# Kernel optimization log

Measured on AMD Instinct MI355X. Metric: run time of the kernel, lower is better.

The kernel has to match this reference:

```python
import jax, jax.numpy as jnp
import numpy as np

N_SRNA, N_MRNA, F, H, E, Q = 20000, 100000, 128, 128, 1000000, 500000


def _sage(x_src, x_dst, src_idx, dst_idx, n_dst, Wl, bl, Wr):
    # PyG SAGEConv: out = lin_l(mean_{j in N(i)} x_j) + lin_r(x_i)
    msg = x_src[src_idx]                                   # [E, F] gather
    agg = jax.ops.segment_sum(msg, dst_idx, num_segments=n_dst)
    cnt = jax.ops.segment_sum(jnp.ones((msg.shape[0],), msg.dtype), dst_idx,
                              num_segments=n_dst)
    mean = agg / jnp.maximum(cnt, 1.0)[:, None]            # [n_dst, F]
    return mean @ Wl + bl + x_dst @ Wr


def setup_inputs() -> dict:
    key = jax.random.key(0)
    ks = jax.random.split(key, 24)
    s = 1.0 / np.sqrt(F)
    inp = {
        'x_srna': jax.random.normal(ks[0], (N_SRNA, F), jnp.float32),
        'x_mrna': jax.random.normal(ks[1], (N_MRNA, F), jnp.float32),
        'src_sm': jax.random.randint(ks[2], (E,), 0, N_SRNA, jnp.int32),
        'dst_sm': jax.random.randint(ks[3], (E,), 0, N_MRNA, jnp.int32),
        'src_ms': jax.random.randint(ks[4], (E,), 0, N_MRNA, jnp.int32),
        'dst_ms': jax.random.randint(ks[5], (E,), 0, N_SRNA, jnp.int32),
        'lbl_row': jax.random.randint(ks[6], (Q,), 0, N_SRNA, jnp.int32),
        'lbl_col': jax.random.randint(ks[7], (Q,), 0, N_MRNA, jnp.int32),
    }
    wnames = ['W1l_sm', 'W1r_sm', 'W1l_ms', 'W1r_ms',
              'W2l_sm', 'W2r_sm', 'W2l_ms', 'W2r_ms']
    for i, n in enumerate(wnames):
        inp[n] = jax.random.normal(ks[8 + i], (F, H), jnp.float32) * s
    for n in ['b1_sm', 'b1_ms', 'b2_sm', 'b2_ms']:
        inp[n] = jnp.zeros((H,), jnp.float32)
    return inp


def reference(x_srna, x_mrna, src_sm, dst_sm, src_ms, dst_ms, lbl_row, lbl_col,
              W1l_sm, b1_sm, W1r_sm, W1l_ms, b1_ms, W1r_ms,
              W2l_sm, b2_sm, W2r_sm, W2l_ms, b2_ms, W2r_ms):
    # Layer 1 (hetero: each dst type receives from exactly one edge type) + ReLU
    h_mrna = jax.nn.relu(_sage(x_srna, x_mrna, src_sm, dst_sm, N_MRNA,
                               W1l_sm, b1_sm, W1r_sm))
    h_srna = jax.nn.relu(_sage(x_mrna, x_srna, src_ms, dst_ms, N_SRNA,
                               W1l_ms, b1_ms, W1r_ms))
    # Layer 2 (no activation)
    z_mrna = _sage(h_srna, h_mrna, src_sm, dst_sm, N_MRNA, W2l_sm, b2_sm, W2r_sm)
    z_srna = _sage(h_mrna, h_srna, src_ms, dst_ms, N_SRNA, W2l_ms, b2_ms, W2r_ms)
    # Edge decoder: dot product over gathered embeddings
    return jnp.sum(z_srna[lbl_row] * z_mrna[lbl_col], axis=-1)
```

## Files before the change

### kernel.cpp

```cpp
#include <hip/hip_runtime.h>

#define N_SRNA  20000
#define N_MRNA  100000
#define FDIM    128
#define NE      1000000
#define NQ      500000
#define NDST_ALL (N_MRNA + N_SRNA)

#define NB_M 196
#define NB_S 157
#define NB   (NB_M + NB_S)
#define NB_Q 196
#define ECAP 8192
#define QCAP 4096

typedef __attribute__((ext_vector_type(8))) short bf16x8;
typedef __attribute__((ext_vector_type(4))) float f32x4;

__device__ __forceinline__ unsigned short f2bf(float f) {
    unsigned int u = __float_as_uint(f);
    unsigned int r = (u + 0x7fffu + ((u >> 16) & 1u)) >> 16;
    return (unsigned short)r;
}
__device__ __forceinline__ float bf2f(unsigned short h) {
    return __uint_as_float((unsigned int)h << 16);
}

__global__ __launch_bounds__(256) void k_bscatter(const int* __restrict__ src_sm,
                                                  const int* __restrict__ dst_sm,
                                                  const int* __restrict__ src_ms,
                                                  const int* __restrict__ dst_ms,
                                                  int* __restrict__ bcur,
                                                  unsigned int* __restrict__ recs) {
    __shared__ int lh[NB], gb[NB], lc[NB];
    int t = threadIdx.x;
    for (int i = t; i < NB; i += 256) { lh[i] = 0; lc[i] = 0; }
    __syncthreads();
    unsigned int rec[16];
    int bk[16];
    int i0 = blockIdx.x * 4096;
#pragma unroll
    for (int j = 0; j < 16; ++j) {
        int i = i0 + j * 256 + t;
        int b = -1; unsigned int r = 0;
        if (i < NE) {
            int d = dst_sm[i];
            b = d >> 9;
            r = ((unsigned int)(d - (b << 9)) << 17) | (unsigned int)src_sm[i];
        } else if (i < 2 * NE) {
            int jj = i - NE;
            int d = dst_ms[jj];
            int bs = d >> 7;
            b = NB_M + bs;
            r = ((unsigned int)(d - (bs << 7)) << 17) | (unsigned int)src_ms[jj];
        }
        bk[j] = b; rec[j] = r;
        if (b >= 0) atomicAdd(&lh[b], 1);
    }
    __syncthreads();
    for (int i = t; i < NB; i += 256)
        gb[i] = lh[i] ? atomicAdd(&bcur[i], lh[i]) : 0;
    __syncthreads();
#pragma unroll
    for (int j = 0; j < 16; ++j) {
        int b = bk[j];
        if (b >= 0) {
            int slot = atomicAdd(&lc[b], 1);
            recs[(size_t)b * ECAP + gb[b] + slot] = rec[j];
        }
    }
}

__global__ __launch_bounds__(256) void k_bbuild(const unsigned int* __restrict__ recs,
                                                const int* __restrict__ bcur,
                                                int* __restrict__ begd,
                                                int* __restrict__ degd,
                                                int* __restrict__ col) {
    __shared__ int lh[512], lptr[512], lps[256];
    const int b = blockIdx.x, t = threadIdx.x;
    const int nd = (b < NB_M) ? min(512, N_MRNA - (b << 9))
                              : min(128, N_SRNA - ((b - NB_M) << 7));
    const int dst0 = (b < NB_M) ? (b << 9) : N_MRNA + ((b - NB_M) << 7);
    const int base = b * ECAP;
    const int nbe = bcur[b];

    lh[t] = 0; lh[t + 256] = 0;
    __syncthreads();
    for (int e = t; e < nbe; e += 256)
        atomicAdd(&lh[recs[(size_t)base + e] >> 17], 1);
    __syncthreads();

    int a0 = lh[2 * t], a1 = lh[2 * t + 1];
    int ps = a0 + a1;
    lps[t] = ps;
    __syncthreads();
    for (int off = 1; off < 256; off <<= 1) {
        int x = (t >= off) ? lps[t - off] : 0;
        __syncthreads();
        lps[t] += x;
        __syncthreads();
    }
    int ex = lps[t] - ps;
    lptr[2 * t] = ex;
    lptr[2 * t + 1] = ex + a0;
    __syncthreads();

    for (int d = t; d < nd; d += 256) {
        begd[dst0 + d] = base + lptr[d];
        degd[dst0 + d] = lh[d];
    }
    __syncthreads();
    lh[t] = lptr[t]; lh[t + 256] = lptr[t + 256];
    __syncthreads();
    for (int e = t; e < nbe; e += 256) {
        unsigned int r = recs[(size_t)base + e];
        int slot = atomicAdd(&lh[r >> 17], 1);
        col[base + slot] = (int)(r & 0x1FFFFu);
    }
}

__global__ __launch_bounds__(256) void k_qscatter(const int* __restrict__ lbl_row,
                                                  const int* __restrict__ lbl_col,
                                                  int* __restrict__ qbcur,
                                                  uint2* __restrict__ qrecs) {
    __shared__ int lh[NB_Q], gb[NB_Q], lc[NB_Q];
    int t = threadIdx.x;
    for (int i = t; i < NB_Q; i += 256) { lh[i] = 0; lc[i] = 0; }
    __syncthreads();
    uint2 rec[16];
    int bk[16];
    int i0 = blockIdx.x * 4096;
#pragma unroll
    for (int j = 0; j < 16; ++j) {
        int i = i0 + j * 256 + t;
        int b = -1; uint2 r = make_uint2(0, 0);
        if (i < NQ) {
            int c = lbl_col[i];
            b = c >> 9;
            r.x = (unsigned int)i;
            r.y = ((unsigned int)(c - (b << 9)) << 15) | (unsigned int)lbl_row[i];
        }
        bk[j] = b; rec[j] = r;
        if (b >= 0) atomicAdd(&lh[b], 1);
    }
    __syncthreads();
    for (int i = t; i < NB_Q; i += 256)
        gb[i] = lh[i] ? atomicAdd(&qbcur[i], lh[i]) : 0;
    __syncthreads();
#pragma unroll
    for (int j = 0; j < 16; ++j) {
        int b = bk[j];
        if (b >= 0) {
            int slot = atomicAdd(&lc[b], 1);
            qrecs[(size_t)b * QCAP + gb[b] + slot] = rec[j];
        }
    }
}

__global__ __launch_bounds__(256) void k_qbbuild(const uint2* __restrict__ qrecs,
                                                 const int* __restrict__ qbcur,
                                                 int* __restrict__ qbeg,
                                                 int* __restrict__ qdeg,
                                                 uint2* __restrict__ qdat) {
    __shared__ int lh[512], lptr[512], lps[256];
    const int b = blockIdx.x, t = threadIdx.x;
    const int nd = min(512, N_MRNA - (b << 9));
    const int col0 = b << 9;
    const int base = b * QCAP;
    const int nbe = qbcur[b];

    lh[t] = 0; lh[t + 256] = 0;
    __syncthreads();
    for (int e = t; e < nbe; e += 256)
        atomicAdd(&lh[qrecs[(size_t)base + e].y >> 15], 1);
    __syncthreads();

    int a0 = lh[2 * t], a1 = lh[2 * t + 1];
    int ps = a0 + a1;
    lps[t] = ps;
    __syncthreads();
    for (int off = 1; off < 256; off <<= 1) {
        int x = (t >= off) ? lps[t - off] : 0;
        __syncthreads();
        lps[t] += x;
        __syncthreads();
    }
    int ex = lps[t] - ps;
    lptr[2 * t] = ex;
    lptr[2 * t + 1] = ex + a0;
    __syncthreads();

    for (int d = t; d < nd; d += 256) {
        qbeg[col0 + d] = base + lptr[d];
        qdeg[col0 + d] = lh[d];
    }
    __syncthreads();
    lh[t] = lptr[t]; lh[t + 256] = lptr[t + 256];
    __syncthreads();
    for (int e = t; e < nbe; e += 256) {
        uint2 r = qrecs[(size_t)base + e];
        int slot = atomicAdd(&lh[r.y >> 15], 1);
        qdat[base + slot] = make_uint2(r.y & 0x7FFFu, r.x);
    }
}

__global__ __launch_bounds__(256) void k_cvt_bf(const float* __restrict__ src,
                                                unsigned short* __restrict__ dst, int n4) {
    int i = blockIdx.x * 256 + threadIdx.x;
    int stride = gridDim.x * 256;
    for (; i < n4; i += stride) {
        float4 v = ((const float4*)src)[i];
        unsigned int p0 = (unsigned int)f2bf(v.x) | ((unsigned int)f2bf(v.y) << 16);
        unsigned int p1 = (unsigned int)f2bf(v.z) | ((unsigned int)f2bf(v.w) << 16);
        ((uint2*)dst)[i] = make_uint2(p0, p1);
    }
}

__global__ __launch_bounds__(256) void k_build_wt4(
        const float* __restrict__ Wl0, const float* __restrict__ Wr0, unsigned short* __restrict__ Wt0,
        const float* __restrict__ Wl1, const float* __restrict__ Wr1, unsigned short* __restrict__ Wt1,
        const float* __restrict__ Wl2, const float* __restrict__ Wr2, unsigned short* __restrict__ Wt2,
        const float* __restrict__ Wl3, const float* __restrict__ Wr3, unsigned short* __restrict__ Wt3) {
    int g = blockIdx.x >> 7;
    const float* Wl; const float* Wr; unsigned short* Wt;
    if (g == 0)      { Wl = Wl0; Wr = Wr0; Wt = Wt0; }
    else if (g == 1) { Wl = Wl1; Wr = Wr1; Wt = Wt1; }
    else if (g == 2) { Wl = Wl2; Wr = Wr2; Wt = Wt2; }
    else             { Wl = Wl3; Wr = Wr3; Wt = Wt3; }
    int tid = (blockIdx.x & 127) * 256 + threadIdx.x;
    int c = tid & 127, k = tid >> 7;
    float v = (k < 128) ? Wl[k * 128 + c] : Wr[(k - 128) * 128 + c];
    Wt[c * 256 + k] = f2bf(v);
}

__global__ __launch_bounds__(256) void k_seg_mean2(const unsigned short* __restrict__ srcA,
                                                   const unsigned short* __restrict__ srcB,
                                                   const int* __restrict__ begd,
                                                   const int* __restrict__ degd,
                                                   const int* __restrict__ cols,
                                                   unsigned short* __restrict__ outA,
                                                   unsigned short* __restrict__ outB,
                                                   int nA, int nTot) {
    int wave = (blockIdx.x * 256 + threadIdx.x) >> 6;
    int l = threadIdx.x & 63;
    if (wave >= nTot) return;
    const int q = l >> 4, lq = l & 15;
    const unsigned short* xs;
    unsigned short* o;
    if (wave < nA) { xs = srcA; o = outA + (size_t)wave * FDIM; }
    else           { xs = srcB; o = outB + (size_t)(wave - nA) * FDIM; }

    int beg = begd[wave], deg = degd[wave];
    float acc[8];
#pragma unroll
    for (int k = 0; k < 8; ++k) acc[k] = 0.f;

    int e = 0;
    for (; e + 8 <= deg; e += 8) {
        int s0 = cols[beg + e + q];
        int s1 = cols[beg + e + 4 + q];
        bf16x8 v0 = *(const bf16x8*)(xs + (size_t)s0 * FDIM + lq * 8);
        bf16x8 v1 = *(const bf16x8*)(xs + (size_t)s1 * FDIM + lq * 8);
#pragma unroll
        for (int k = 0; k < 8; ++k) acc[k] += bf2f((unsigned short)v0[k]);
#pragma unroll
        for (int k = 0; k < 8; ++k) acc[k] += bf2f((unsigned short)v1[k]);
    }
    for (; e < deg; e += 4) {
        bool valid = (e + q) < deg;
        int idx = beg + min(e + q, max(deg - 1, 0));
        int s = cols[idx];
        bf16x8 v = *(const bf16x8*)(xs + (size_t)s * FDIM + lq * 8);
        if (valid) {
#pragma unroll
            for (int k = 0; k < 8; ++k) acc[k] += bf2f((unsigned short)v[k]);
        }
    }
#pragma unroll
    for (int k = 0; k < 8; ++k) {
        acc[k] += __shfl_xor(acc[k], 16);
        acc[k] += __shfl_xor(acc[k], 32);
    }
    if (q == 0) {
        float inv = 1.0f / fmaxf((float)deg, 1.0f);
        uint4 pv;
        pv.x = (unsigned int)f2bf(acc[0] * inv) | ((unsigned int)f2bf(acc[1] * inv) << 16);
        pv.y = (unsigned int)f2bf(acc[2] * inv) | ((unsigned int)f2bf(acc[3] * inv) << 16);
        pv.z = (unsigned int)f2bf(acc[4] * inv) | ((unsigned int)f2bf(acc[5] * inv) << 16);
        pv.w = (unsigned int)f2bf(acc[6] * inv) | ((unsigned int)f2bf(acc[7] * inv) << 16);
        ((uint4*)o)[lq] = pv;
    }
}

template <bool RELU>
__global__ __launch_bounds__(256, 2) void k_gemm_mfma2(
        const unsigned short* __restrict__ A0a, const unsigned short* __restrict__ A1a,
        const unsigned short* __restrict__ Wta, const float* __restrict__ biasa,
        unsigned short* __restrict__ outa, int na, int nblka,
        const unsigned short* __restrict__ A0b, const unsigned short* __restrict__ A1b,
        const unsigned short* __restrict__ Wtb, const float* __restrict__ biasb,
        unsigned short* __restrict__ outb, int nb) {
    __shared__ uint4 smem4[4352];
    char* smem = (char*)smem4;

    const unsigned short *A0, *A1, *Wt;
    const float* bias;
    unsigned short* out;
    int n, bid;
    if ((int)blockIdx.x < nblka) {
        A0 = A0a; A1 = A1a; Wt = Wta; bias = biasa; out = outa; n = na; bid = blockIdx.x;
    } else {
        A0 = A0b; A1 = A1b; Wt = Wtb; bias = biasb; out = outb; n = nb; bid = blockIdx.x - nblka;
    }

    const int t = threadIdx.x;
#pragma unroll
    for (int i = 0; i < 16; ++i) {
        int j = i * 256 + t;
        int byteo = j << 4;
        int c = byteo >> 9;
        int off = byteo & 511;
        int swz = off ^ ((c & 7) << 4);
        uint4 v = ((const uint4*)Wt)[j];
        *(uint4*)(smem + c * 512 + swz) = v;
    }
    __syncthreads();

    const int w = t >> 6, l = t & 63;
    const int wr = w >> 1, wc = w & 1;
    const int rowbase = bid * 128 + wr * 64;
    const int colbase = wc * 64;
    const int lr = l & 15;
    const int lk = (l >> 4) * 8;

    f32x4 acc[4][4];
#pragma unroll
    for (int a = 0; a < 4; ++a)
#pragma unroll
        for (int b = 0; b < 4; ++b)
#pragma unroll
            for (int e = 0; e < 4; ++e) acc[a][b][e] = 0.f;

    bf16x8 az;
#pragma unroll
    for (int e = 0; e < 8; ++e) az[e] = 0;

#pragma unroll
    for (int s = 0; s < 8; ++s) {
        const unsigned short* Abuf = (s < 4) ? A0 : A1;
        const int kk = (s & 3) * 32 + lk;
        bf16x8 afr[4];
#pragma unroll
        for (int af = 0; af < 4; ++af) {
            int row = rowbase + af * 16 + lr;
            afr[af] = (row < n) ? *(const bf16x8*)(Abuf + (size_t)row * FDIM + kk) : az;
        }
        bf16x8 bfr[4];
#pragma unroll
        for (int bf = 0; bf < 4; ++bf) {
            int c = colbase + bf * 16 + lr;
            int off = s * 64 + lk * 2;
            int swz = off ^ ((c & 7) << 4);
            bfr[bf] = *(const bf16x8*)(smem + c * 512 + swz);
        }
#pragma unroll
        for (int af = 0; af < 4; ++af)
#pragma unroll
            for (int bf = 0; bf < 4; ++bf)
                acc[af][bf] = __builtin_amdgcn_mfma_f32_16x16x32_bf16(afr[af], bfr[bf],
                                                                      acc[af][bf], 0, 0, 0);
    }

    __syncthreads();
    float* sD = (float*)(smem + w * 17408);

#pragma unroll
    for (int af = 0; af < 4; ++af)
#pragma unroll
        for (int bf = 0; bf < 4; ++bf)
#pragma unroll
            for (int r = 0; r < 4; ++r)
                sD[(af * 16 + (l >> 4) * 4 + r) * 68 + bf * 16 + lr] = acc[af][bf][r];

#pragma unroll
    for (int j = 0; j < 8; ++j) {
        int flat = j * 512 + l * 8;
        int row = flat >> 6;
        int c0 = flat & 63;
        int grow = rowbase + row;
        if (grow >= n) continue;
        float4 v0 = *(float4*)(&sD[row * 68 + c0]);
        float4 v1 = *(float4*)(&sD[row * 68 + c0 + 4]);
        int gc = colbase + c0;
        float4 b0 = *(const float4*)(bias + gc);
        float4 b1 = *(const float4*)(bias + gc + 4);
        float o[8] = {v0.x + b0.x, v0.y + b0.y, v0.z + b0.z, v0.w + b0.w,
                      v1.x + b1.x, v1.y + b1.y, v1.z + b1.z, v1.w + b1.w};
        if (RELU) {
#pragma unroll
            for (int e = 0; e < 8; ++e) o[e] = fmaxf(o[e], 0.f);
        }
        uint4 pv;
        pv.x = (unsigned int)f2bf(o[0]) | ((unsigned int)f2bf(o[1]) << 16);
        pv.y = (unsigned int)f2bf(o[2]) | ((unsigned int)f2bf(o[3]) << 16);
        pv.z = (unsigned int)f2bf(o[4]) | ((unsigned int)f2bf(o[5]) << 16);
        pv.w = (unsigned int)f2bf(o[6]) | ((unsigned int)f2bf(o[7]) << 16);
        *(uint4*)(out + (size_t)grow * FDIM + gc) = pv;
    }
}

__global__ __launch_bounds__(256) void k_decoder_csr(const unsigned short* __restrict__ zS,
                                                     const unsigned short* __restrict__ zM,
                                                     const int* __restrict__ qbeg,
                                                     const int* __restrict__ qdeg,
                                                     const uint2* __restrict__ qdat,
                                                     float* __restrict__ out) {
    int c = (blockIdx.x * 256 + threadIdx.x) >> 6;
    int l = threadIdx.x & 63;
    if (c >= N_MRNA) return;
    int cnt = qdeg[c];
    if (cnt == 0) return;
    int beg = qbeg[c];
    const int q = l >> 4, lq = l & 15;

    bf16x8 vm = *(const bf16x8*)(zM + (size_t)c * FDIM + lq * 8);
    float mxf[8];
#pragma unroll
    for (int k = 0; k < 8; ++k) mxf[k] = bf2f((unsigned short)vm[k]);

    for (int e = 0; e < cnt; e += 4) {
        bool valid = (e + q) < cnt;
        int idx = beg + min(e + q, cnt - 1);
        uint2 d = qdat[idx];
        bf16x8 va = *(const bf16x8*)(zS + (size_t)d.x * FDIM + lq * 8);
        float s = 0.f;
#pragma unroll
        for (int k = 0; k < 8; ++k) s += bf2f((unsigned short)va[k]) * mxf[k];
        s += __shfl_xor(s, 1);
        s += __shfl_xor(s, 2);
        s += __shfl_xor(s, 4);
        s += __shfl_xor(s, 8);
        if (valid && lq == 0) out[d.y] = s;
    }
}

extern "C" void kernel_launch(void* const* d_in, const int* in_sizes, int n_in,
                              void* d_out, int out_size, void* d_ws, size_t ws_size,
                              hipStream_t stream) {
    const float* x_srna = (const float*)d_in[0];
    const float* x_mrna = (const float*)d_in[1];
    const int* src_sm = (const int*)d_in[2];
    const int* dst_sm = (const int*)d_in[3];
    const int* src_ms = (const int*)d_in[4];
    const int* dst_ms = (const int*)d_in[5];
    const int* lbl_row = (const int*)d_in[6];
    const int* lbl_col = (const int*)d_in[7];
    const float* W1l_sm = (const float*)d_in[8];
    const float* W1r_sm = (const float*)d_in[9];
    const float* W1l_ms = (const float*)d_in[10];
    const float* W1r_ms = (const float*)d_in[11];
    const float* W2l_sm = (const float*)d_in[12];
    const float* W2r_sm = (const float*)d_in[13];
    const float* W2l_ms = (const float*)d_in[14];
    const float* W2r_ms = (const float*)d_in[15];
    const float* b1_sm = (const float*)d_in[16];
    const float* b1_ms = (const float*)d_in[17];
    const float* b2_sm = (const float*)d_in[18];
    const float* b2_ms = (const float*)d_in[19];
    float* out = (float*)d_out;

    char* ws = (char*)d_ws;
    unsigned short* xS_bf   = (unsigned short*)(ws + 0);
    unsigned short* xM_bf   = (unsigned short*)(ws + 5120000);
    unsigned short* meanM   = (unsigned short*)(ws + 30720000);
    unsigned short* meanS   = (unsigned short*)(ws + 56320000);
    unsigned short* hM_bf   = (unsigned short*)(ws + 61440000);
    unsigned short* hS_bf   = (unsigned short*)(ws + 87040000);
    unsigned short* Wt1sm   = (unsigned short*)(ws + 92160000);
    unsigned short* Wt1ms   = (unsigned short*)(ws + 92225536);
    unsigned short* Wt2sm   = (unsigned short*)(ws + 92291072);
    unsigned short* Wt2ms   = (unsigned short*)(ws + 92356608);
    int* begd               = (int*)(ws + 92422144);
    int* degd               = (int*)(ws + 92902144);
    int* col_all            = (int*)(ws + 93382144);
    unsigned int* recs      = (unsigned int*)(ws + 104949248);
    uint2* qrecs            = (uint2*)(ws + 116516352);
    uint2* qdat             = (uint2*)(ws + 122938880);
    int* qbeg               = (int*)(ws + 129361408);
    int* qdeg               = (int*)(ws + 129761408);
    int* bcur               = (int*)(ws + 130161408);
    int* qbcur              = (int*)(ws + 130162820);

    k_cvt_bf<<<2048, 256, 0, stream>>>(x_srna, xS_bf, N_SRNA * FDIM / 4);
    k_cvt_bf<<<2048, 256, 0, stream>>>(x_mrna, xM_bf, N_MRNA * FDIM / 4);
    k_build_wt4<<<512, 256, 0, stream>>>(W1l_sm, W1r_sm, Wt1sm,
                                         W1l_ms, W1r_ms, Wt1ms,
                                         W2l_sm, W2r_sm, Wt2sm,
                                         W2l_ms, W2r_ms, Wt2ms);

    hipMemsetAsync(bcur, 0, (NB + NB_Q) * sizeof(int), stream);

    const int nblk = (2 * NE + 4095) / 4096;
    k_bscatter<<<nblk, 256, 0, stream>>>(src_sm, dst_sm, src_ms, dst_ms, bcur, recs);
    k_bbuild<<<NB, 256, 0, stream>>>(recs, bcur, begd, degd, col_all);

    const int nqblk = (NQ + 4095) / 4096;
    k_qscatter<<<nqblk, 256, 0, stream>>>(lbl_row, lbl_col, qbcur, qrecs);
    k_qbbuild<<<NB_Q, 256, 0, stream>>>(qrecs, qbcur, qbeg, qdeg, qdat);

    const int nblk_m = (N_MRNA + 127) / 128;
    const int nblk_s = (N_SRNA + 127) / 128;
    const int segblk = (NDST_ALL * 64 + 255) / 256;

    k_seg_mean2<<<segblk, 256, 0, stream>>>(xS_bf, xM_bf, begd, degd, col_all,
                                            meanM, meanS, N_MRNA, NDST_ALL);
    k_gemm_mfma2<true><<<nblk_m + nblk_s, 256, 0, stream>>>(
        meanM, xM_bf, Wt1sm, b1_sm, hM_bf, N_MRNA, nblk_m,
        meanS, xS_bf, Wt1ms, b1_ms, hS_bf, N_SRNA);

    k_seg_mean2<<<segblk, 256, 0, stream>>>(hS_bf, hM_bf, begd, degd, col_all,
                                            meanM, meanS, N_MRNA, NDST_ALL);
    k_gemm_mfma2<false><<<nblk_m + nblk_s, 256, 0, stream>>>(
        meanM, hM_bf, Wt2sm, b2_sm, meanM, N_MRNA, nblk_m,
        meanS, hS_bf, Wt2ms, b2_ms, meanS, N_SRNA);

    k_decoder_csr<<<(N_MRNA + 3) / 4, 256, 0, stream>>>(meanS, meanM, qbeg, qdeg, qdat, out);
}
```

Measured before the change: 449.4 us.

## Merge preprocessing launches and map one quarter-wave per row in segment mean

Fuses the edge and query scatter kernels into one launch, the two bucket-build kernels into one, and the two fp32-to-bf16 conversions into one, to cut launch count and let independent work share the GPU. The segment-mean kernel now gives each 16-lane group its own destination row (four rows per wave) instead of a whole wave per row. Each group walks its edges serially with a 4-wide unroll, which removes the cross-lane shuffle reduction. This raises row-level parallelism but gives less memory-level parallelism per row and more divergence between groups whose degrees differ.

```diff
diff --git a/kernel.cpp b/kernel.cpp
--- a/kernel.cpp
+++ b/kernel.cpp
@@ -13,6 +13,8 @@
 #define NB_Q 196
 #define ECAP 8192
 #define QCAP 4096
+#define NBLK_E 489
+#define NBLK_Q 123
 
 typedef __attribute__((ext_vector_type(8))) short bf16x8;
 typedef __attribute__((ext_vector_type(4))) float f32x4;
@@ -26,193 +28,205 @@
     return __uint_as_float((unsigned int)h << 16);
 }
 
-__global__ __launch_bounds__(256) void k_bscatter(const int* __restrict__ src_sm,
-                                                  const int* __restrict__ dst_sm,
-                                                  const int* __restrict__ src_ms,
-                                                  const int* __restrict__ dst_ms,
-                                                  int* __restrict__ bcur,
-                                                  unsigned int* __restrict__ recs) {
+__global__ __launch_bounds__(256) void k_scatter_all(const int* __restrict__ src_sm,
+                                                     const int* __restrict__ dst_sm,
+                                                     const int* __restrict__ src_ms,
+                                                     const int* __restrict__ dst_ms,
+                                                     const int* __restrict__ lbl_row,
+                                                     const int* __restrict__ lbl_col,
+                                                     int* __restrict__ bcur,
+                                                     int* __restrict__ qbcur,
+                                                     unsigned int* __restrict__ recs,
+                                                     uint2* __restrict__ qrecs) {
     __shared__ int lh[NB], gb[NB], lc[NB];
     int t = threadIdx.x;
-    for (int i = t; i < NB; i += 256) { lh[i] = 0; lc[i] = 0; }
-    __syncthreads();
-    unsigned int rec[16];
-    int bk[16];
-    int i0 = blockIdx.x * 4096;
-#pragma unroll
-    for (int j = 0; j < 16; ++j) {
-        int i = i0 + j * 256 + t;
-        int b = -1; unsigned int r = 0;
-        if (i < NE) {
-            int d = dst_sm[i];
-            b = d >> 9;
-            r = ((unsigned int)(d - (b << 9)) << 17) | (unsigned int)src_sm[i];
-        } else if (i < 2 * NE) {
-            int jj = i - NE;
-            int d = dst_ms[jj];
-            int bs = d >> 7;
-            b = NB_M + bs;
-            r = ((unsigned int)(d - (bs << 7)) << 17) | (unsigned int)src_ms[jj];
-        }
-        bk[j] = b; rec[j] = r;
-        if (b >= 0) atomicAdd(&lh[b], 1);
-    }
-    __syncthreads();
-    for (int i = t; i < NB; i += 256)
-        gb[i] = lh[i] ? atomicAdd(&bcur[i], lh[i]) : 0;
-    __syncthreads();
-#pragma unroll
-    for (int j = 0; j < 16; ++j) {
-        int b = bk[j];
-        if (b >= 0) {
-            int slot = atomicAdd(&lc[b], 1);
-            recs[(size_t)b * ECAP + gb[b] + slot] = rec[j];
-        }
-    }
-}
-
-__global__ __launch_bounds__(256) void k_bbuild(const unsigned int* __restrict__ recs,
-                                                const int* __restrict__ bcur,
-                                                int* __restrict__ begd,
-                                                int* __restrict__ degd,
-                                                int* __restrict__ col) {
+    if ((int)blockIdx.x < NBLK_E) {
+        for (int i = t; i < NB; i += 256) { lh[i] = 0; lc[i] = 0; }
+        __syncthreads();
+        unsigned int rec[16];
+        int bk[16];
+        int i0 = blockIdx.x * 4096;
+#pragma unroll
+        for (int j = 0; j < 16; ++j) {
+            int i = i0 + j * 256 + t;
+            int b = -1; unsigned int r = 0;
+            if (i < NE) {
+                int d = dst_sm[i];
+                b = d >> 9;
+                r = ((unsigned int)(d - (b << 9)) << 17) | (unsigned int)src_sm[i];
+            } else if (i < 2 * NE) {
+                int jj = i - NE;
+                int d = dst_ms[jj];
+                int bs = d >> 7;
+                b = NB_M + bs;
+                r = ((unsigned int)(d - (bs << 7)) << 17) | (unsigned int)src_ms[jj];
+            }
+            bk[j] = b; rec[j] = r;
+            if (b >= 0) atomicAdd(&lh[b], 1);
+        }
+        __syncthreads();
+        for (int i = t; i < NB; i += 256)
+            gb[i] = lh[i] ? atomicAdd(&bcur[i], lh[i]) : 0;
+        __syncthreads();
+#pragma unroll
+        for (int j = 0; j < 16; ++j) {
+            int b = bk[j];
+            if (b >= 0) {
+                int slot = atomicAdd(&lc[b], 1);
+                recs[(size_t)b * ECAP + gb[b] + slot] = rec[j];
+            }
+        }
+    } else {
+        for (int i = t; i < NB_Q; i += 256) { lh[i] = 0; lc[i] = 0; }
+        __syncthreads();
+        uint2 rec[16];
+        int bk[16];
+        int i0 = ((int)blockIdx.x - NBLK_E) * 4096;
+#pragma unroll
+        for (int j = 0; j < 16; ++j) {
+            int i = i0 + j * 256 + t;
+            int b = -1; uint2 r = make_uint2(0, 0);
+            if (i < NQ) {
+                int c = lbl_col[i];
+                b = c >> 9;
+                r.x = (unsigned int)i;
+                r.y = ((unsigned int)(c - (b << 9)) << 15) | (unsigned int)lbl_row[i];
+            }
+            bk[j] = b; rec[j] = r;
+            if (b >= 0) atomicAdd(&lh[b], 1);
+        }
+        __syncthreads();
+        for (int i = t; i < NB_Q; i += 256)
+            gb[i] = lh[i] ? atomicAdd(&qbcur[i], lh[i]) : 0;
+        __syncthreads();
+#pragma unroll
+        for (int j = 0; j < 16; ++j) {
+            int b = bk[j];
+            if (b >= 0) {
+                int slot = atomicAdd(&lc[b], 1);
+                qrecs[(size_t)b * QCAP + gb[b] + slot] = rec[j];
+            }
+        }
+    }
+}
+
+__global__ __launch_bounds__(256) void k_build_all(const unsigned int* __restrict__ recs,
+                                                   const int* __restrict__ bcur,
+                                                   const uint2* __restrict__ qrecs,
+                                                   const int* __restrict__ qbcur,
+                                                   int* __restrict__ begd,
+                                                   int* __restrict__ degd,
+                                                   int* __restrict__ col,
+                                                   int* __restrict__ qbeg,
+                                                   int* __restrict__ qdeg,
+                                                   uint2* __restrict__ qdat) {
     __shared__ int lh[512], lptr[512], lps[256];
-    const int b = blockIdx.x, t = threadIdx.x;
-    const int nd = (b < NB_M) ? min(512, N_MRNA - (b << 9))
-                              : min(128, N_SRNA - ((b - NB_M) << 7));
-    const int dst0 = (b < NB_M) ? (b << 9) : N_MRNA + ((b - NB_M) << 7);
-    const int base = b * ECAP;
-    const int nbe = bcur[b];
-
-    lh[t] = 0; lh[t + 256] = 0;
-    __syncthreads();
-    for (int e = t; e < nbe; e += 256)
-        atomicAdd(&lh[recs[(size_t)base + e] >> 17], 1);
-    __syncthreads();
-
-    int a0 = lh[2 * t], a1 = lh[2 * t + 1];
-    int ps = a0 + a1;
-    lps[t] = ps;
-    __syncthreads();
-    for (int off = 1; off < 256; off <<= 1) {
-        int x = (t >= off) ? lps[t - off] : 0;
-        __syncthreads();
-        lps[t] += x;
-        __syncthreads();
-    }
-    int ex = lps[t] - ps;
-    lptr[2 * t] = ex;
-    lptr[2 * t + 1] = ex + a0;
-    __syncthreads();
-
-    for (int d = t; d < nd; d += 256) {
-        begd[dst0 + d] = base + lptr[d];
-        degd[dst0 + d] = lh[d];
-    }
-    __syncthreads();
-    lh[t] = lptr[t]; lh[t + 256] = lptr[t + 256];
-    __syncthreads();
-    for (int e = t; e < nbe; e += 256) {
-        unsigned int r = recs[(size_t)base + e];
-        int slot = atomicAdd(&lh[r >> 17], 1);
-        col[base + slot] = (int)(r & 0x1FFFFu);
-    }
-}
-
-__global__ __launch_bounds__(256) void k_qscatter(const int* __restrict__ lbl_row,
-                                                  const int* __restrict__ lbl_col,
-                                                  int* __restrict__ qbcur,
-                                                  uint2* __restrict__ qrecs) {
-    __shared__ int lh[NB_Q], gb[NB_Q], lc[NB_Q];
-    int t = threadIdx.x;
-    for (int i = t; i < NB_Q; i += 256) { lh[i] = 0; lc[i] = 0; }
-    __syncthreads();
-    uint2 rec[16];
-    int bk[16];
-    int i0 = blockIdx.x * 4096;
-#pragma unroll
-    for (int j = 0; j < 16; ++j) {
-        int i = i0 + j * 256 + t;
-        int b = -1; uint2 r = make_uint2(0, 0);
-        if (i < NQ) {
-            int c = lbl_col[i];
-            b = c >> 9;
-            r.x = (unsigned int)i;
-            r.y = ((unsigned int)(c - (b << 9)) << 15) | (unsigned int)lbl_row[i];
-        }
-        bk[j] = b; rec[j] = r;
-        if (b >= 0) atomicAdd(&lh[b], 1);
-    }
-    __syncthreads();
-    for (int i = t; i < NB_Q; i += 256)
-        gb[i] = lh[i] ? atomicAdd(&qbcur[i], lh[i]) : 0;
-    __syncthreads();
-#pragma unroll
-    for (int j = 0; j < 16; ++j) {
-        int b = bk[j];
-        if (b >= 0) {
-            int slot = atomicAdd(&lc[b], 1);
-            qrecs[(size_t)b * QCAP + gb[b] + slot] = rec[j];
-        }
-    }
-}
-
-__global__ __launch_bounds__(256) void k_qbbuild(const uint2* __restrict__ qrecs,
-                                                 const int* __restrict__ qbcur,
-                                                 int* __restrict__ qbeg,
-                                                 int* __restrict__ qdeg,
-                                                 uint2* __restrict__ qdat) {
-    __shared__ int lh[512], lptr[512], lps[256];
-    const int b = blockIdx.x, t = threadIdx.x;
-    const int nd = min(512, N_MRNA - (b << 9));
-    const int col0 = b << 9;
-    const int base = b * QCAP;
-    const int nbe = qbcur[b];
-
-    lh[t] = 0; lh[t + 256] = 0;
-    __syncthreads();
-    for (int e = t; e < nbe; e += 256)
-        atomicAdd(&lh[qrecs[(size_t)base + e].y >> 15], 1);
-    __syncthreads();
-
-    int a0 = lh[2 * t], a1 = lh[2 * t + 1];
-    int ps = a0 + a1;
-    lps[t] = ps;
-    __syncthreads();
-    for (int off = 1; off < 256; off <<= 1) {
-        int x = (t >= off) ? lps[t - off] : 0;
-        __syncthreads();
-        lps[t] += x;
-        __syncthreads();
-    }
-    int ex = lps[t] - ps;
-    lptr[2 * t] = ex;
-    lptr[2 * t + 1] = ex + a0;
-    __syncthreads();
-
-    for (int d = t; d < nd; d += 256) {
-        qbeg[col0 + d] = base + lptr[d];
-        qdeg[col0 + d] = lh[d];
-    }
-    __syncthreads();
-    lh[t] = lptr[t]; lh[t + 256] = lptr[t + 256];
-    __syncthreads();
-    for (int e = t; e < nbe; e += 256) {
-        uint2 r = qrecs[(size_t)base + e];
-        int slot = atomicAdd(&lh[r.y >> 15], 1);
-        qdat[base + slot] = make_uint2(r.y & 0x7FFFu, r.x);
-    }
-}
-
-__global__ __launch_bounds__(256) void k_cvt_bf(const float* __restrict__ src,
-                                                unsigned short* __restrict__ dst, int n4) {
+    const int t = threadIdx.x;
+    if ((int)blockIdx.x < NB) {
+        const int b = blockIdx.x;
+        const int nd = (b < NB_M) ? min(512, N_MRNA - (b << 9))
+                                  : min(128, N_SRNA - ((b - NB_M) << 7));
+        const int dst0 = (b < NB_M) ? (b << 9) : N_MRNA + ((b - NB_M) << 7);
+        const int base = b * ECAP;
+        const int nbe = bcur[b];
+
+        lh[t] = 0; lh[t + 256] = 0;
+        __syncthreads();
+        for (int e = t; e < nbe; e += 256)
+            atomicAdd(&lh[recs[(size_t)base + e] >> 17], 1);
+        __syncthreads();
+
+        int a0 = lh[2 * t], a1 = lh[2 * t + 1];
+        int ps = a0 + a1;
+        lps[t] = ps;
+        __syncthreads();
+        for (int off = 1; off < 256; off <<= 1) {
+            int x = (t >= off) ? lps[t - off] : 0;
+            __syncthreads();
+            lps[t] += x;
+            __syncthreads();
+        }
+        int ex = lps[t] - ps;
+        lptr[2 * t] = ex;
+        lptr[2 * t + 1] = ex + a0;
+        __syncthreads();
+
+        for (int d = t; d < nd; d += 256) {
+            begd[dst0 + d] = base + lptr[d];
+            degd[dst0 + d] = lh[d];
+        }
+        __syncthreads();
+        lh[t] = lptr[t]; lh[t + 256] = lptr[t + 256];
+        __syncthreads();
+        for (int e = t; e < nbe; e += 256) {
+            unsigned int r = recs[(size_t)base + e];
+            int slot = atomicAdd(&lh[r >> 17], 1);
+            col[base + slot] = (int)(r & 0x1FFFFu);
+        }
+    } else {
+        const int b = blockIdx.x - NB;
+        const int nd = min(512, N_MRNA - (b << 9));
+        const int col0 = b << 9;
+        const int base = b * QCAP;
+        const int nbe = qbcur[b];
+
+        lh[t] = 0; lh[t + 256] = 0;
+        __syncthreads();
+        for (int e = t; e < nbe; e += 256)
+            atomicAdd(&lh[qrecs[(size_t)base + e].y >> 15], 1);
+        __syncthreads();
+
+        int a0 = lh[2 * t], a1 = lh[2 * t + 1];
+        int ps = a0 + a1;
+        lps[t] = ps;
+        __syncthreads();
+        for (int off = 1; off < 256; off <<= 1) {
+            int x = (t >= off) ? lps[t - off] : 0;
+            __syncthreads();
+            lps[t] += x;
+            __syncthreads();
+        }
+        int ex = lps[t] - ps;
+        lptr[2 * t] = ex;
+        lptr[2 * t + 1] = ex + a0;
+        __syncthreads();
+
+        for (int d = t; d < nd; d += 256) {
+            qbeg[col0 + d] = base + lptr[d];
+            qdeg[col0 + d] = lh[d];
+        }
+        __syncthreads();
+        lh[t] = lptr[t]; lh[t + 256] = lptr[t + 256];
+        __syncthreads();
+        for (int e = t; e < nbe; e += 256) {
+            uint2 r = qrecs[(size_t)base + e];
+            int slot = atomicAdd(&lh[r.y >> 15], 1);
+            qdat[base + slot] = make_uint2(r.y & 0x7FFFu, r.x);
+        }
+    }
+}
+
+__global__ __launch_bounds__(256) void k_cvt_all(const float* __restrict__ xs,
+                                                 const float* __restrict__ xm,
+                                                 unsigned short* __restrict__ oS,
+                                                 unsigned short* __restrict__ oM) {
+    const int nS4 = N_SRNA * FDIM / 4;
+    const int nT4 = NDST_ALL * FDIM / 4;
     int i = blockIdx.x * 256 + threadIdx.x;
     int stride = gridDim.x * 256;
-    for (; i < n4; i += stride) {
-        float4 v = ((const float4*)src)[i];
-        unsigned int p0 = (unsigned int)f2bf(v.x) | ((unsigned int)f2bf(v.y) << 16);
-        unsigned int p1 = (unsigned int)f2bf(v.z) | ((unsigned int)f2bf(v.w) << 16);
-        ((uint2*)dst)[i] = make_uint2(p0, p1);
+    for (; i < nT4; i += stride) {
+        if (i < nS4) {
+            float4 v = ((const float4*)xs)[i];
+            unsigned int p0 = (unsigned int)f2bf(v.x) | ((unsigned int)f2bf(v.y) << 16);
+            unsigned int p1 = (unsigned int)f2bf(v.z) | ((unsigned int)f2bf(v.w) << 16);
+            ((uint2*)oS)[i] = make_uint2(p0, p1);
+        } else {
+            int j = i - nS4;
+            float4 v = ((const float4*)xm)[j];
+            unsigned int p0 = (unsigned int)f2bf(v.x) | ((unsigned int)f2bf(v.y) << 16);
+            unsigned int p1 = (unsigned int)f2bf(v.z) | ((unsigned int)f2bf(v.w) << 16);
+            ((uint2*)oM)[j] = make_uint2(p0, p1);
+        }
     }
 }
 
@@ -243,45 +257,47 @@
                                                    int nA, int nTot) {
     int wave = (blockIdx.x * 256 + threadIdx.x) >> 6;
     int l = threadIdx.x & 63;
-    if (wave >= nTot) return;
     const int q = l >> 4, lq = l & 15;
-    const unsigned short* xs;
-    unsigned short* o;
-    if (wave < nA) { xs = srcA; o = outA + (size_t)wave * FDIM; }
-    else           { xs = srcB; o = outB + (size_t)(wave - nA) * FDIM; }
-
-    int beg = begd[wave], deg = degd[wave];
+    int r = wave * 4 + q;
+    bool rowok = r < nTot;
+    int rr = rowok ? r : 0;
+    const unsigned short* xs = (rr < nA) ? srcA : srcB;
+    unsigned short* o = (rr < nA) ? (outA + (size_t)rr * FDIM)
+                                  : (outB + (size_t)(rr - nA) * FDIM);
+    int beg = begd[rr];
+    int deg = rowok ? degd[rr] : 0;
+
     float acc[8];
 #pragma unroll
     for (int k = 0; k < 8; ++k) acc[k] = 0.f;
 
     int e = 0;
-    for (; e + 8 <= deg; e += 8) {
-        int s0 = cols[beg + e + q];
-        int s1 = cols[beg + e + 4 + q];
+    for (; e + 4 <= deg; e += 4) {
+        int s0 = cols[beg + e];
+        int s1 = cols[beg + e + 1];
+        int s2 = cols[beg + e + 2];
+        int s3 = cols[beg + e + 3];
         bf16x8 v0 = *(const bf16x8*)(xs + (size_t)s0 * FDIM + lq * 8);
         bf16x8 v1 = *(const bf16x8*)(xs + (size_t)s1 * FDIM + lq * 8);
+        bf16x8 v2 = *(const bf16x8*)(xs + (size_t)s2 * FDIM + lq * 8);
+        bf16x8 v3 = *(const bf16x8*)(xs + (size_t)s3 * FDIM + lq * 8);
 #pragma unroll
         for (int k = 0; k < 8; ++k) acc[k] += bf2f((unsigned short)v0[k]);
 #pragma unroll
         for (int k = 0; k < 8; ++k) acc[k] += bf2f((unsigned short)v1[k]);
-    }
-    for (; e < deg; e += 4) {
-        bool valid = (e + q) < deg;
-        int idx = beg + min(e + q, max(deg - 1, 0));
-        int s = cols[idx];
+#pragma unroll
+        for (int k = 0; k < 8; ++k) acc[k] += bf2f((unsigned short)v2[k]);
+#pragma unroll
+        for (int k = 0; k < 8; ++k) acc[k] += bf2f((unsigned short)v3[k]);
+    }
+    for (; e < deg; ++e) {
+        int s = cols[beg + e];
         bf16x8 v = *(const bf16x8*)(xs + (size_t)s * FDIM + lq * 8);
-        if (valid) {
-#pragma unroll
-            for (int k = 0; k < 8; ++k) acc[k] += bf2f((unsigned short)v[k]);
-        }
-    }
-#pragma unroll
-    for (int k = 0; k < 8; ++k) {
-        acc[k] += __shfl_xor(acc[k], 16);
-        acc[k] += __shfl_xor(acc[k], 32);
-    }
-    if (q == 0) {
+#pragma unroll
+        for (int k = 0; k < 8; ++k) acc[k] += bf2f((unsigned short)v[k]);
+    }
+
+    if (rowok) {
         float inv = 1.0f / fmaxf((float)deg, 1.0f);
         uint4 pv;
         pv.x = (unsigned int)f2bf(acc[0] * inv) | ((unsigned int)f2bf(acc[1] * inv) << 16);
@@ -491,8 +507,7 @@
     int* bcur               = (int*)(ws + 130161408);
     int* qbcur              = (int*)(ws + 130162820);
 
-    k_cvt_bf<<<2048, 256, 0, stream>>>(x_srna, xS_bf, N_SRNA * FDIM / 4);
-    k_cvt_bf<<<2048, 256, 0, stream>>>(x_mrna, xM_bf, N_MRNA * FDIM / 4);
+    k_cvt_all<<<2048, 256, 0, stream>>>(x_srna, x_mrna, xS_bf, xM_bf);
     k_build_wt4<<<512, 256, 0, stream>>>(W1l_sm, W1r_sm, Wt1sm,
                                          W1l_ms, W1r_ms, Wt1ms,
                                          W2l_sm, W2r_sm, Wt2sm,
@@ -500,17 +515,15 @@
 
     hipMemsetAsync(bcur, 0, (NB + NB_Q) * sizeof(int), stream);
 
-    const int nblk = (2 * NE + 4095) / 4096;
-    k_bscatter<<<nblk, 256, 0, stream>>>(src_sm, dst_sm, src_ms, dst_ms, bcur, recs);
-    k_bbuild<<<NB, 256, 0, stream>>>(recs, bcur, begd, degd, col_all);
-
-    const int nqblk = (NQ + 4095) / 4096;
-    k_qscatter<<<nqblk, 256, 0, stream>>>(lbl_row, lbl_col, qbcur, qrecs);
-    k_qbbuild<<<NB_Q, 256, 0, stream>>>(qrecs, qbcur, qbeg, qdeg, qdat);
+    k_scatter_all<<<NBLK_E + NBLK_Q, 256, 0, stream>>>(src_sm, dst_sm, src_ms, dst_ms,
+                                                       lbl_row, lbl_col, bcur, qbcur,
+                                                       recs, qrecs);
+    k_build_all<<<NB + NB_Q, 256, 0, stream>>>(recs, bcur, qrecs, qbcur,
+                                               begd, degd, col_all, qbeg, qdeg, qdat);
 
     const int nblk_m = (N_MRNA + 127) / 128;
     const int nblk_s = (N_SRNA + 127) / 128;
-    const int segblk = (NDST_ALL * 64 + 255) / 256;
+    const int segblk = (NDST_ALL + 15) / 16;
 
     k_seg_mean2<<<segblk, 256, 0, stream>>>(xS_bf, xM_bf, begd, degd, col_all,
                                             meanM, meanS, N_MRNA, NDST_ALL);
```

New measurement: 411.4 us. 8.4% less time.
